# Kernel optimization log

Hardware: AMD Instinct MI355X
Metric: run time of the kernel (lower is better)

## Reference

```python
import jax, jax.numpy as jnp
import numpy as np

N, E = 50000, 800000
IN_CH, HID, OUT_CH = 128, 256, 40
L, R = 3, 16
EPS = 1e-12


def setup_inputs() -> dict:
    key = jax.random.key(0)
    ks = jax.random.split(key, 16)
    s = 0.05
    return {
        'x': jax.random.normal(ks[0], (N, IN_CH), jnp.float32),
        'edge_index': jax.random.randint(ks[1], (2, E), 0, N, dtype=jnp.int64),
        'W_in': jax.random.normal(ks[2], (IN_CH, HID), jnp.float32) * s,
        'b_in': jnp.zeros((HID,), jnp.float32),
        'centers': jax.random.normal(ks[3], (L, R, HID), jnp.float32),
        'log_sigma': jnp.zeros((L, R, HID), jnp.float32),
        'W_rule': jax.random.normal(ks[4], (L, R, HID, HID), jnp.float32) * s,
        'b_rule': jnp.zeros((L, R, HID), jnp.float32),
        'W_self': jax.random.normal(ks[5], (L, HID, HID), jnp.float32) * s,
        'b_self': jnp.zeros((L, HID), jnp.float32),
        'gamma': jnp.ones((L, HID), jnp.float32),
        'beta': jnp.zeros((L, HID), jnp.float32),
        'W_h1': jax.random.normal(ks[6], (HID, HID // 2), jnp.float32) * s,
        'b_h1': jnp.zeros((HID // 2,), jnp.float32),
        'W_h2': jax.random.normal(ks[7], (HID // 2, OUT_CH), jnp.float32) * s,
        'b_h2': jnp.zeros((OUT_CH,), jnp.float32),
    }


def membership(h, c, log_s):
    # Gaussian rule firing, expanded to matmuls to avoid [N,R,H] distance tensor
    inv_s2 = jnp.exp(-2.0 * log_s)                         # [R,H]
    d = (h * h) @ inv_s2.T - 2.0 * (h @ (c * inv_s2).T) \
        + jnp.sum(c * c * inv_s2, axis=-1)                 # [N,R]
    firing = jnp.exp(-0.5 * d)
    return firing / (jnp.sum(firing, axis=-1, keepdims=True) + EPS)


def fmpl(h, src, dst, c, log_s, W_r, b_r, W_s, b_s):
    n = h.shape[0]
    deg = jax.ops.segment_sum(jnp.ones(src.shape[0], h.dtype), dst, num_segments=n)
    agg = jax.ops.segment_sum(h[src], dst, num_segments=n) / jnp.clip(deg, 1.0)[:, None]
    mu = membership(h, c, log_s)                           # [N,R]
    per_rule = jnp.einsum('ni,rio->nro', agg, W_r) + b_r[None]  # [N,R,H]
    fuzzy = jnp.einsum('nr,nro->no', mu, per_rule)
    return h @ W_s + b_s + fuzzy


def batchnorm(x, g, b, eps=1e-5):
    m = jnp.mean(x, axis=0)
    v = jnp.var(x, axis=0)
    return (x - m) * jax.lax.rsqrt(v + eps) * g + b


def reference(x, edge_index, W_in, b_in, centers, log_sigma, W_rule, b_rule,
              W_self, b_self, gamma, beta, W_h1, b_h1, W_h2, b_h2):
    src, dst = edge_index[0], edge_index[1]
    h = jax.nn.relu(x @ W_in + b_in)                       # dropout = identity (eval)
    for l in range(L):
        h_new = fmpl(h, src, dst, centers[l], log_sigma[l], W_rule[l], b_rule[l],
                     W_self[l], b_self[l])
        h_new = jax.nn.relu(batchnorm(h_new, gamma[l], beta[l]))
        h = h + h_new
    logits = jax.nn.relu(h @ W_h1 + b_h1) @ W_h2 + b_h2
    return jax.nn.softmax(logits, axis=-1)
```

## Files before the change

kernel.cpp:

```cpp
#include <hip/hip_runtime.h>
#include <hip/hip_fp16.h>
#include <cstdint>
#include <cstddef>

using u16 = unsigned short;
using u32 = unsigned int;

typedef _Float16 half8 __attribute__((ext_vector_type(8)));
typedef float f32x4 __attribute__((ext_vector_type(4)));

static inline int cdiv(int a, int b) { return (a + b - 1) / b; }


__global__ void prep_k(const float* __restrict__ Wr,
                       const float* __restrict__ Ws, const float* __restrict__ br,
                       const float* __restrict__ W_in, const float* __restrict__ W_h1,
                       const float* __restrict__ W_h2,
                       const float* __restrict__ centers, const float* __restrict__ logsig,
                       u16* __restrict__ wcat,
                       u16* __restrict__ winp, u16* __restrict__ wh1p,
                       u16* __restrict__ wh2p,
                       u16* __restrict__ pcB, float* __restrict__ pccc,
                       int* __restrict__ zerobase, int nzero,
                       int Z, int Wb) {
    const int bid = blockIdx.x;
    const int tid = threadIdx.x;
    if (bid < Z) {
        int i = bid * 256 + tid;
        if (i < nzero) zerobase[i] = 0;
        return;
    }
    if (bid < Z + Wb) {
        size_t t = (size_t)(bid - Z) * 256 + tid;
        const size_t PL = 552u * 256u * 8u;
        int l = (int)(t / PL);
        size_t rem = t - (size_t)l * PL;
        int kp = (int)(rem >> 11);
        int o = (int)((rem >> 3) & 255);
        int e = (int)(rem & 7);
        int k = kp * 8 + e;
        float v;
        if (k < 4096)      v = Wr[((((size_t)l * 16 + (k >> 8)) * 256) + (k & 255)) * 256 + o];
        else if (k < 4352) v = Ws[(((size_t)l * 256) + (k - 4096)) * 256 + o];
        else if (k < 4368) v = br[(((size_t)l * 16) + (k - 4352)) * 256 + o];
        else               v = 0.f;
        union { u16 u; _Float16 h; } c; c.h = (_Float16)v;
        wcat[t] = c.u;
        return;
    }
    if (bid < Z + Wb + 128) {
        size_t t = (size_t)(bid - Z - Wb) * 256 + tid;
        int e = (int)(t & 7), o = (int)((t >> 3) & 255);
        int kp = (int)(t >> 11);
        union { u16 u; _Float16 h; } c; c.h = (_Float16)W_in[(size_t)(kp * 8 + e) * 256 + o];
        winp[t] = c.u;
        return;
    }
    if (bid < Z + Wb + 256) {
        size_t t = (size_t)(bid - Z - Wb - 128) * 256 + tid;
        int e = (int)(t & 7), o = (int)((t >> 3) & 127);
        int kp = (int)(t >> 10);
        union { u16 u; _Float16 h; } c; c.h = (_Float16)W_h1[(size_t)(kp * 8 + e) * 128 + o];
// ... 52 lines not shown
        for (int e = blockIdx.x * 256 + tid; e < E; e += 256 * 256)
            atomicAdd(&deg[dst[e]], 1);
        gbar(1);
        if (blockIdx.x == 0) {
            const int chunk = (n + 255) >> 8;
            int s0 = tid * chunk, s1 = s0 + chunk; if (s1 > n) s1 = n; if (s0 > n) s0 = n;
            int tot = 0;
            for (int i = s0; i < s1; ++i) tot += atomicAdd(&deg[i], 0);
            __shared__ int sm[256];
            sm[tid] = tot; __syncthreads();
            for (int off = 1; off < 256; off <<= 1) {
                int t = (tid >= off) ? sm[tid - off] : 0;
                __syncthreads(); sm[tid] += t; __syncthreads();
            }
            int base = sm[tid] - tot;
            for (int i = s0; i < s1; ++i) {
                int d = atomicAdd(&deg[i], 0);
                indptr[i] = base; cursor[i] = base;
                deginv[i] = 1.f / (float)(d > 1 ? d : 1);
                base += d;
            }
            if (tid == 255) indptr[n] = sm[255];
        }
        gbar(2);
        for (int e = blockIdx.x * 256 + tid; e < E; e += 256 * 256) {
            int d = dst[e];
            int pos = atomicAdd(&cursor[d], 1);
            ssrc[pos] = src[e];
        }
        gbar(3);
        if (blockIdx.x == 0 && tid == 0) *done = 1;
    }
    int lane = tid & 63, wave = tid >> 6;
    for (int node = blockIdx.x * 4 + wave; node < n; node += 256 * 4) {
        if (bflag[node >> 7] == 0) continue;
        int j0 = indptr[node], j1 = indptr[node + 1];
        float a0 = 0, a1 = 0, a2 = 0, a3 = 0;
        for (int j = j0; j < j1; ++j) {
            int sN = ssrc[j];
            union { uint2 u; _Float16 h[4]; } hv;
            hv.u = *(const uint2*)(h16 + (size_t)sN * 256 + lane * 4);
            a0 += (float)hv.h[0]; a1 += (float)hv.h[1];
            a2 += (float)hv.h[2]; a3 += (float)hv.h[3];
        }
        float di = deginv[node];
        union { uint2 u; _Float16 h[4]; } o;
        o.h[0] = (_Float16)(a0 * di); o.h[1] = (_Float16)(a1 * di);
        o.h[2] = (_Float16)(a2 * di); o.h[3] = (_Float16)(a3 * di);
        *(uint2*)(agg16 + (size_t)node * 256 + lane * 4) = o.u;
    }
}


template <int MODE, int NCHUNK>
__launch_bounds__(256, 2)
__global__ void gemm_mn(const u16* __restrict__ A, const u16* __restrict__ A2,
                        const u16* __restrict__ MU, const u16* __restrict__ Bp,
                        const float* __restrict__ bias, const int* __restrict__ bflag,
                        u16* __restrict__ outH, float* __restrict__ bnsum,
                        const u16* __restrict__ pcB, const float* __restrict__ pccc,
                        u16* __restrict__ mu16, int* __restrict__ bflagN,
                        int nrows) {
    __shared__ __align__(16) u16 lds[24576];
    __shared__ float bnbuf[2048];
    u16* lA = lds;
    u16* lB = lds + 8192;
    const int tid = threadIdx.x;
    const int row0 = blockIdx.x * 128;
    const int lane = tid & 63;
    const int q = lane >> 4, mm = lane & 15;
    const int wave = tid >> 6;

    f32x4 acc[2][16];
#pragma unroll
    for (int i = 0; i < 2; ++i)
#pragma unroll
        for (int j = 0; j < 16; ++j) acc[i][j] = (f32x4){0.f, 0.f, 0.f, 0.f};

    int cb = 0, cbEnd = NCHUNK;
    if (MODE == 1 && bflag[blockIdx.x] == 0) { cb = 64; cbEnd = 68; }

    for (; cb < cbEnd; ++cb) {
#pragma unroll
        for (int it = 0; it < 8; ++it) {
            int idx = it * 256 + tid;
            int p = idx >> 8, col = idx & 255;
            uint4 v = *(const uint4*)(Bp + (((size_t)(cb * 8 + p)) * 256 + col) * 8);
            *(uint4*)(lB + (size_t)idx * 8) = v;
        }
#pragma unroll
        for (int it = 0; it < 4; ++it) {
            int idx = it * 256 + tid;
            int p = idx >> 7, row = idx & 127;
            int grow = row0 + row; if (grow >= nrows) grow = nrows - 1;
            uint4 v;
            if (MODE == 0) {
                const float* xr = (const float*)A + (size_t)grow * 128 + cb * 64 + (p << 3);
                float4 f0 = *(const float4*)xr;
                float4 f1 = *(const float4*)(xr + 4);
                union { uint4 u4; _Float16 h[8]; } cv;
                cv.h[0] = (_Float16)f0.x; cv.h[1] = (_Float16)f0.y;
                cv.h[2] = (_Float16)f0.z; cv.h[3] = (_Float16)f0.w;
                cv.h[4] = (_Float16)f1.x; cv.h[5] = (_Float16)f1.y;
                cv.h[6] = (_Float16)f1.z; cv.h[7] = (_Float16)f1.w;
                v = cv.u4;
            } else {
                if (cb < 64) {
                    int r = cb >> 2;
                    int i0 = ((cb & 3) << 6) + (p << 3);
                    v = *(const uint4*)(A + (size_t)grow * 256 + i0);
                    union { u16 u; _Float16 h; } mu; mu.u = MU[(size_t)grow * 16 + r];
                    union { uint4 u4; _Float16 h[8]; } wv; wv.u4 = v;
#pragma unroll
                    for (int j = 0; j < 8; ++j) wv.h[j] = wv.h[j] * mu.h;
                    v = wv.u4;
                } else if (cb < 68) {
                    int i0 = ((cb - 64) << 6) + (p << 3);
                    v = *(const uint4*)(A2 + (size_t)grow * 256 + i0);
                } else {
                    int j0 = p << 3;
                    if (j0 < 16) v = *(const uint4*)(MU + (size_t)grow * 16 + j0);
                    else v = (uint4){0, 0, 0, 0};
                }
            }
            *(uint4*)(lA + (size_t)idx * 8) = v;
        }
        __syncthreads();
#pragma unroll
        for (int kc = 0; kc < 2; ++kc) {
            int pp = kc * 4 + q;
            half8 af0 = *(const half8*)(lA + ((size_t)pp * 128 + wave * 32 + mm) * 8);
            half8 af1 = *(const half8*)(lA + ((size_t)pp * 128 + wave * 32 + 16 + mm) * 8);
#pragma unroll
            for (int nt = 0; nt < 16; ++nt) {
                half8 bf = *(const half8*)(lB + ((size_t)pp * 256 + nt * 16 + mm) * 8);
                acc[0][nt] = __builtin_amdgcn_mfma_f32_16x16x32_f16(af0, bf, acc[0][nt], 0, 0, 0);
                acc[1][nt] = __builtin_amdgcn_mfma_f32_16x16x32_f16(af1, bf, acc[1][nt], 0, 0, 0);
            }
        }
        __syncthreads();
    }

    int nr = nrows - row0; if (nr > 128) nr = 128;

    if (MODE == 1) {
#pragma unroll
        for (int nt = 0; nt < 16; ++nt) {
            int cl = nt * 16 + mm;
            float bb = bias[cl];
            float s = 0.f, ss = 0.f;
#pragma unroll
            for (int mt = 0; mt < 2; ++mt) {
#pragma unroll
                for (int r = 0; r < 4; ++r) {
                    int row = wave * 32 + mt * 16 + q * 4 + r;
                    float v = acc[mt][nt][r] + bb;
                    if (row < nr) { s += v; ss += v * v; }
                }
            }
            s += __shfl_xor(s, 16);  s += __shfl_xor(s, 32);
            ss += __shfl_xor(ss, 16); ss += __shfl_xor(ss, 32);
            if (q == 0) {
                bnbuf[(wave * 256 + cl) * 2 + 0] = s;
                bnbuf[(wave * 256 + cl) * 2 + 1] = ss;
            }
        }
        __syncthreads();
        {
            float s  = bnbuf[tid * 2]     + bnbuf[(256 + tid) * 2]
                     + bnbuf[(512 + tid) * 2] + bnbuf[(768 + tid) * 2];
            float ss = bnbuf[tid * 2 + 1] + bnbuf[(256 + tid) * 2 + 1]
                     + bnbuf[(512 + tid) * 2 + 1] + bnbuf[(768 + tid) * 2 + 1];
            atomicAdd(&bnsum[tid], s);
            atomicAdd(&bnsum[256 + tid], ss);
        }
    }

    f32x4 macc0 = (f32x4){0.f, 0.f, 0.f, 0.f};
    f32x4 macc1 = (f32x4){0.f, 0.f, 0.f, 0.f};
#pragma unroll
    for (int h = 0; h < 2; ++h) {
        __syncthreads();
#pragma unroll
        for (int nt = 0; nt < 8; ++nt) {
            int cl = h * 128 + nt * 16 + mm;
            float bb = bias[cl];
#pragma unroll
            for (int mt = 0; mt < 2; ++mt) {
#pragma unroll
                for (int r = 0; r < 4; ++r) {
                    int row = wave * 32 + mt * 16 + q * 4 + r;
                    float v = acc[mt][h * 8 + nt][r] + bb;
                    if (MODE == 0) v = fmaxf(v, 0.f);
                    union { u16 u; _Float16 hh; } cc; cc.hh = (_Float16)v;
                    lds[row * 136 + nt * 16 + mm] = cc.u;
                }
            }
        }
        __syncthreads();
#pragma unroll
        for (int it = 0; it < 8; ++it) {
            int idx = it * 256 + tid;
            int row = idx >> 4, cp = idx & 15;
            if (row < nr) {
                uint4 v = *(const uint4*)(lds + row * 136 + cp * 8);
                *(uint4*)(outH + (size_t)(row0 + row) * 256 + h * 128 + cp * 8) = v;
            }
        }
        if (MODE == 0) {
            const u16* brow = pcB + (size_t)mm * 512;
#pragma unroll
            for (int it2 = 0; it2 < 4; ++it2) {
                int lk = it2 * 32 + q * 8;
                half8 b1 = *(const half8*)(brow + h * 128 + lk);
                half8 b2 = *(const half8*)(brow + 256 + h * 128 + lk);
                half8 a0 = *(const half8*)(lds + ((size_t)(wave * 32 + mm)) * 136 + lk);
                half8 a1 = *(const half8*)(lds + ((size_t)(wave * 32 + 16 + mm)) * 136 + lk);
                macc0 = __builtin_amdgcn_mfma_f32_16x16x32_f16(a0 * a0, b1, macc0, 0, 0, 0);
                macc0 = __builtin_amdgcn_mfma_f32_16x16x32_f16(a0, b2, macc0, 0, 0, 0);
                macc1 = __builtin_amdgcn_mfma_f32_16x16x32_f16(a1 * a1, b1, macc1, 0, 0, 0);
                macc1 = __builtin_amdgcn_mfma_f32_16x16x32_f16(a1, b2, macc1, 0, 0, 0);
            }
        }
    }

    if (MODE == 0) {
        float cc = pccc[mm];
        bool any = false;
#pragma unroll
        for (int g = 0; g < 2; ++g) {
            f32x4 macc = g ? macc1 : macc0;
#pragma unroll
            for (int r = 0; r < 4; ++r) {
                float d = macc[r] + cc;
                float f = expf(-0.5f * d);
                float s = f;
                s += __shfl_xor(s, 1); s += __shfl_xor(s, 2);
                s += __shfl_xor(s, 4); s += __shfl_xor(s, 8);
                int node = row0 + (wave * 2 + g) * 16 + q * 4 + r;
                if (node < nrows) {
                    union { u16 u; _Float16 hh; } c2;
                    c2.hh = (_Float16)(f / (s + 1e-12f));
                    mu16[(size_t)node * 16 + mm] = c2.u;
                    if (c2.u != 0) any = true;
                }
            }
        }
        if (__any(any) && lane == 0) {
            atomicOr(&bflagN[blockIdx.x], 1);
            atomicOr(&bflagN[511], 1);
        }
    }
}


template <int DOMEMB>
__launch_bounds__(256)
__global__ void updmemb_k(const u16* __restrict__ pre16, const float* __restrict__ bnsum,
                          const float* __restrict__ gamma, const float* __restrict__ beta,
                          u16* __restrict__ h16,
                          const u16* __restrict__ pcB, const float* __restrict__ pccc,
                          u16* __restrict__ mu16, int* __restrict__ bflag, int n) {
    const int tid = threadIdx.x;
    __shared__ float l_ab[512];
    {
        float su = bnsum[tid];
        float sq = bnsum[256 + tid];
        float invn = 1.f / (float)n;
        float m = su * invn;
        float al = gamma[tid] * rsqrtf(sq * invn - m * m + 1e-5f);
        l_ab[tid] = al;
        l_ab[256 + tid] = beta[tid] - m * al;
    }
    __syncthreads();

    const int lane = tid & 63, wave = tid >> 6;
    const int q = lane >> 4, mm = lane & 15;
    const int n0 = (blockIdx.x * 4 + wave) * 16;
    if (n0 >= n) return;
    const int node = n0 + mm;
    const bool valid = node < n;
    const int nodeC = valid ? node : n - 1;
    const size_t base = (size_t)nodeC * 256 + q * 8;

    half8 v16[8];
#pragma unroll
    for (int b = 0; b < 8; ++b) {
        int c = b * 32 + q * 8;
        float4 alA = *(const float4*)(l_ab + c);
        float4 alB = *(const float4*)(l_ab + c + 4);
        float4 shA = *(const float4*)(l_ab + 256 + c);
        float4 shB = *(const float4*)(l_ab + 256 + c + 4);
        float aarr[8] = {alA.x, alA.y, alA.z, alA.w, alB.x, alB.y, alB.z, alB.w};
        float harr[8] = {shA.x, shA.y, shA.z, shA.w, shB.x, shB.y, shB.z, shB.w};
        union { uint4 u; _Float16 hh[8]; } p, hv, o;
        p.u  = *(const uint4*)(pre16 + base + b * 32);
        hv.u = *(const uint4*)(h16 + base + b * 32);
#pragma unroll
        for (int j = 0; j < 8; ++j) {
            float v = (float)hv.hh[j] + fmaxf((float)p.hh[j] * aarr[j] + harr[j], 0.f);
            o.hh[j] = (_Float16)v;
        }
        if (valid) *(uint4*)(h16 + base + b * 32) = o.u;
        v16[b] = *(half8*)&o;
    }

    if (DOMEMB) {
        const u16* brow = pcB + (size_t)mm * 512;
        f32x4 acc = (f32x4){0.f, 0.f, 0.f, 0.f};
#pragma unroll
        for (int it = 0; it < 16; ++it) {
            half8 a = v16[it & 7];
            if (it < 8) a = a * a;
            half8 bb = *(const half8*)(brow + it * 32 + q * 8);
            acc = __builtin_amdgcn_mfma_f32_16x16x32_f16(a, bb, acc, 0, 0, 0);
        }
        float cc = pccc[mm];
        bool any = false;
#pragma unroll
        for (int r = 0; r < 4; ++r) {
            float d = acc[r] + cc;
            float f = expf(-0.5f * d);
            float s = f;
            s += __shfl_xor(s, 1); s += __shfl_xor(s, 2);
            s += __shfl_xor(s, 4); s += __shfl_xor(s, 8);
            int nd = n0 + q * 4 + r;
            if (nd < n) {
                union { u16 u; _Float16 h; } c2;
                c2.h = (_Float16)(f / (s + 1e-12f));
                mu16[(size_t)nd * 16 + mm] = c2.u;
                if (c2.u != 0) any = true;
            }
        }
        if (__any(any) && lane == 0) {
            atomicOr(&bflag[n0 >> 7], 1);
            atomicOr(&bflag[511], 1);
        }
    }
}


__launch_bounds__(256, 4)
__global__ void head_k(const u16* __restrict__ A, const u16* __restrict__ Bp,
                       const float* __restrict__ bias,
                       const u16* __restrict__ wh2, const float* __restrict__ bh2,
                       float* __restrict__ outF, int nrows) {
    __shared__ __align__(16) u16 lds[17408];
    u16* lA = lds;
    u16* lB = lds + 8192;
    const int tid = threadIdx.x;
    const int row0 = blockIdx.x * 128;
    const int lane = tid & 63;
    const int q = lane >> 4, mm = lane & 15;
    const int wave = tid >> 6;
    const int wm = wave >> 1, wn = wave & 1;

    f32x4 acc[4][4];
#pragma unroll
    for (int i = 0; i < 4; ++i)
#pragma unroll
        for (int j = 0; j < 4; ++j) acc[i][j] = (f32x4){0.f, 0.f, 0.f, 0.f};

    for (int cb = 0; cb < 4; ++cb) {
#pragma unroll
        for (int it = 0; it < 4; ++it) {
            int idx = it * 256 + tid;
            int p = idx >> 7, col = idx & 127;
            uint4 v = *(const uint4*)(Bp + (((size_t)(cb * 8 + p)) * 128 + col) * 8);
            *(uint4*)(lB + (size_t)idx * 8) = v;
        }
#pragma unroll
        for (int it = 0; it < 4; ++it) {
            int idx = it * 256 + tid;
            int p = idx >> 7, row = idx & 127;
            int grow = row0 + row; if (grow >= nrows) grow = nrows - 1;
            uint4 v = *(const uint4*)(A + (size_t)grow * 256 + cb * 64 + p * 8);
            *(uint4*)(lA + (size_t)idx * 8) = v;
        }
        __syncthreads();
#pragma unroll
        for (int kc = 0; kc < 2; ++kc) {
            int pp = kc * 4 + q;
            half8 af[4], bf[4];
#pragma unroll
            for (int mt = 0; mt < 4; ++mt)
                af[mt] = *(const half8*)(lA + ((size_t)pp * 128 + wm * 64 + mt * 16 + mm) * 8);
#pragma unroll
            for (int nt = 0; nt < 4; ++nt)
                bf[nt] = *(const half8*)(lB + ((size_t)pp * 128 + wn * 64 + nt * 16 + mm) * 8);
#pragma unroll
            for (int mt = 0; mt < 4; ++mt)
#pragma unroll
                for (int nt = 0; nt < 4; ++nt)
                    acc[mt][nt] = __builtin_amdgcn_mfma_f32_16x16x32_f16(af[mt], bf[nt], acc[mt][nt], 0, 0, 0);
        }
        __syncthreads();
    }

#pragma unroll
    for (int nt = 0; nt < 4; ++nt) {
        const int cl = wn * 64 + nt * 16 + mm;
#pragma unroll
        for (int mt = 0; mt < 4; ++mt) {
#pragma unroll
            for (int r = 0; r < 4; ++r) {
                int row = wm * 64 + mt * 16 + q * 4 + r;
                float v = fmaxf(acc[mt][nt][r] + bias[cl], 0.f);
                union { u16 u; _Float16 h; } cc; cc.h = (_Float16)v;
                lds[row * 136 + cl] = cc.u;
            }
        }
    }
    __syncthreads();

    const bool c2ok = (mm < 8);
    float b0 = bh2[mm], b1 = bh2[16 + mm];
    float b2 = c2ok ? bh2[32 + mm] : 0.f;
#pragma unroll
    for (int half = 0; half < 2; ++half) {
        int rbase = half * 64 + wave * 16;
        f32x4 hacc[3];
#pragma unroll
        for (int t = 0; t < 3; ++t) hacc[t] = (f32x4){0.f, 0.f, 0.f, 0.f};
#pragma unroll
        for (int c = 0; c < 4; ++c) {
            half8 a = *(const half8*)(lds + (rbase + mm) * 136 + c * 32 + q * 8);
#pragma unroll
            for (int t = 0; t < 3; ++t) {
                half8 b = *(const half8*)(wh2 + ((size_t)(c * 4 + q) * 48 + t * 16 + mm) * 8);
                hacc[t] = __builtin_amdgcn_mfma_f32_16x16x32_f16(a, b, hacc[t], 0, 0, 0);
            }
        }
#pragma unroll
        for (int r = 0; r < 4; ++r) {
            int node = row0 + rbase + q * 4 + r;
            float v0 = hacc[0][r] + b0;
            float v1 = hacc[1][r] + b1;
            float v2 = c2ok ? (hacc[2][r] + b2) : -3e38f;
            float m = fmaxf(fmaxf(v0, v1), v2);
            m = fmaxf(m, __shfl_xor(m, 1)); m = fmaxf(m, __shfl_xor(m, 2));
            m = fmaxf(m, __shfl_xor(m, 4)); m = fmaxf(m, __shfl_xor(m, 8));
            float e0 = expf(v0 - m), e1 = expf(v1 - m);
            float e2 = c2ok ? expf(v2 - m) : 0.f;
            float s = e0 + e1 + e2;
            s += __shfl_xor(s, 1); s += __shfl_xor(s, 2);
            s += __shfl_xor(s, 4); s += __shfl_xor(s, 8);
            float is = 1.f / s;
            if (node < nrows) {
                float* op = outF + (size_t)node * 40;
                op[mm] = e0 * is;
                op[16 + mm] = e1 * is;
                if (c2ok) op[32 + mm] = e2 * is;
            }
        }
    }
}


extern "C" void kernel_launch(void* const* d_in, const int* in_sizes, int n_in,
                              void* d_out, int out_size, void* d_ws, size_t ws_size,
                              hipStream_t stream) {
    const float* x       = (const float*)d_in[0];
    const int*   ei      = (const int*)d_in[1];
    const float* W_in    = (const float*)d_in[2];
    const float* b_in    = (const float*)d_in[3];
    const float* centers = (const float*)d_in[4];
    const float* logsig  = (const float*)d_in[5];
    const float* W_rule  = (const float*)d_in[6];
    const float* b_rule  = (const float*)d_in[7];
    const float* W_self  = (const float*)d_in[8];
    const float* b_self  = (const float*)d_in[9];
    const float* gamma   = (const float*)d_in[10];
    const float* beta    = (const float*)d_in[11];
    const float* W_h1    = (const float*)d_in[12];
    const float* b_h1    = (const float*)d_in[13];
    const float* W_h2    = (const float*)d_in[14];
    const float* b_h2    = (const float*)d_in[15];

    const int N = in_sizes[0] / 128;
    const int E = in_sizes[1] / 2;
    const int* e_src = ei;
    const int* e_dst = ei + E;

    char* w = (char*)d_ws;
    size_t off = 0;
    auto alloc = [&](size_t bytes) -> void* {
        void* p = w + off;
        off = (off + bytes + 255) & ~(size_t)255;
        return p;
    };

    const int gx = cdiv(N, 128);

    u16*   h16    = (u16*)  alloc((size_t)N * 256 * 2);
    u16*   pre16  = (u16*)  alloc((size_t)N * 256 * 2);
    u16*   agg16  = (u16*)  alloc((size_t)N * 256 * 2);
    u16*   mu16   = (u16*)  alloc((size_t)N * 16 * 2);
    u16*   wcat   = (u16*)  alloc((size_t)3 * 552 * 256 * 8 * 2);
    u16*   winp   = (u16*)  alloc((size_t)16 * 256 * 8 * 2);
    u16*   wh1p   = (u16*)  alloc((size_t)32 * 128 * 8 * 2);
    u16*   wh2p   = (u16*)  alloc((size_t)16 * 48 * 8 * 2);
    u16*   pcB    = (u16*)  alloc((size_t)48 * 512 * 2);
    float* pccc   = (float*)alloc((size_t)48 * 4);
    int*   indptr = (int*)  alloc((size_t)(N + 1) * 4);
    int*   cursor = (int*)  alloc((size_t)N * 4);
    float* deginv = (float*)alloc((size_t)N * 4);
    int*   ssrc   = (int*)  alloc((size_t)E * 4);
    const int nzero = N + 3 * 512 + 3 * 512 + 16;
    int*   zerob  = (int*)  alloc((size_t)nzero * 4);
    int*   deg    = zerob;
    int*   bflagA = zerob + N;
    float* bnsumA = (float*)(zerob + N + 3 * 512);
    int*   misc   = zerob + N + 3 * 512 + 3 * 512;
    int*   done   = misc;
    int*   csrctr = misc + 1;

    const int Z = cdiv(nzero, 256);
    const int Wb = 3 * 552 * 256 * 8 / 256;
    const int prep_grid = Z + Wb + 128 + 128 + 24 + 48;

    prep_k<<<prep_grid, 256, 0, stream>>>(W_rule, W_self, b_rule, W_in, W_h1, W_h2,
                                          centers, logsig, wcat, winp, wh1p, wh2p,
                                          pcB, pccc, zerob, nzero, Z, Wb);

    gemm_mn<0, 2><<<gx, 256, 0, stream>>>((const u16*)x, nullptr, nullptr, winp,
                                          b_in, nullptr, h16, nullptr,
                                          pcB, pccc, mu16, bflagA, N);

    for (int l = 0; l < 3; ++l) {
        int* bf = bflagA + l * 512;
        float* bns = bnsumA + l * 512;
        csr_agg_g<<<256, 256, 0, stream>>>(e_src, e_dst, deg, indptr, cursor, deginv,
                                           ssrc, csrctr, bf, done, h16, agg16, E, N);
        gemm_mn<1, 69><<<gx, 256, 0, stream>>>(agg16, h16, mu16,
                                               wcat + (size_t)l * 552 * 256 * 8,
                                               b_self + l * 256, bf, pre16, bns,
                                               nullptr, nullptr, nullptr, nullptr, N);
        if (l < 2) {
            updmemb_k<1><<<cdiv(N, 64), 256, 0, stream>>>(pre16, bns, gamma + l * 256,
                                                          beta + l * 256, h16,
                                                          pcB + (size_t)(l + 1) * 16 * 512,
                                                          pccc + (l + 1) * 16, mu16,
                                                          bflagA + (l + 1) * 512, N);
        } else {
            updmemb_k<0><<<cdiv(N, 64), 256, 0, stream>>>(pre16, bns, gamma + l * 256,
                                                          beta + l * 256, h16,
                                                          nullptr, nullptr, nullptr,
                                                          nullptr, N);
        }
    }

    head_k<<<gx, 256, 0, stream>>>(h16, wh1p, b_h1, wh2p, b_h2, (float*)d_out, N);
}
```

Before: 310.3 us.

## Drop LDS staging in fuzzy GEMM and fuse head MLP into last BN update

The main GEMM now has each wave load its A fragments straight from global memory and read B fragments directly from the pre-packed weights, with no shared-memory staging and no block barriers. LDS becomes a small per-wave tile used only for the epilogue, and occupancy is raised to three blocks per SM. The separate head kernel is removed, and the final batchnorm/residual kernel computes the two head matmuls and the softmax on its in-register tile, which also skips writing h back. The trade-off is that B is reloaded from global/L2 by every wave rather than shared through LDS, which adds memory traffic.

```diff
diff --git a/kernel.cpp b/kernel.cpp
--- a/kernel.cpp
+++ b/kernel.cpp
@@ -8,6 +8,8 @@
 
 typedef _Float16 half8 __attribute__((ext_vector_type(8)));
 typedef float f32x4 __attribute__((ext_vector_type(4)));
+
+#define MF(a, b, c) __builtin_amdgcn_mfma_f32_16x16x32_f16((a), (b), (c), 0, 0, 0)
 
 static inline int cdiv(int a, int b) { return (a + b - 1) / b; }
 
@@ -166,24 +168,24 @@
 }
 
 
-template <int MODE, int NCHUNK>
-__launch_bounds__(256, 2)
-__global__ void gemm_mn(const u16* __restrict__ A, const u16* __restrict__ A2,
-                        const u16* __restrict__ MU, const u16* __restrict__ Bp,
-                        const float* __restrict__ bias, const int* __restrict__ bflag,
-                        u16* __restrict__ outH, float* __restrict__ bnsum,
-                        const u16* __restrict__ pcB, const float* __restrict__ pccc,
-                        u16* __restrict__ mu16, int* __restrict__ bflagN,
-                        int nrows) {
-    __shared__ __align__(16) u16 lds[24576];
+template <int MODE>
+__launch_bounds__(256, 3)
+__global__ void gemm_d(const float* __restrict__ xf, const u16* __restrict__ hg,
+                       const u16* __restrict__ agg, const u16* __restrict__ mu,
+                       const u16* __restrict__ Bp, const float* __restrict__ bias,
+                       const int* __restrict__ bflag,
+                       u16* __restrict__ outH, float* __restrict__ bnl,
+                       const u16* __restrict__ pcB, const float* __restrict__ pccc,
+                       u16* __restrict__ mu16o, int* __restrict__ bflagN, int n) {
+    __shared__ __align__(16) u16 tiles[4][4352];
     __shared__ float bnbuf[2048];
-    u16* lA = lds;
-    u16* lB = lds + 8192;
-    const int tid = threadIdx.x;
-    const int row0 = blockIdx.x * 128;
-    const int lane = tid & 63;
-    const int q = lane >> 4, mm = lane & 15;
-    const int wave = tid >> 6;
+    const int tid = threadIdx.x, bid = blockIdx.x;
+    const int row0 = bid * 128;
+    const int lane = tid & 63, q = lane >> 4, mm = lane & 15, wave = tid >> 6;
+    u16* tw = tiles[wave];
+    int nr = n - row0; if (nr > 128) nr = 128;
+    int g0 = row0 + wave * 32 + mm;      if (g0 >= n) g0 = n - 1;
+    int g1 = row0 + wave * 32 + 16 + mm; if (g1 >= n) g1 = n - 1;
 
     f32x4 acc[2][16];
 #pragma unroll
@@ -191,25 +193,14 @@
 #pragma unroll
         for (int j = 0; j < 16; ++j) acc[i][j] = (f32x4){0.f, 0.f, 0.f, 0.f};
 
-    int cb = 0, cbEnd = NCHUNK;
-    if (MODE == 1 && bflag[blockIdx.x] == 0) { cb = 64; cbEnd = 68; }
-
-    for (; cb < cbEnd; ++cb) {
-#pragma unroll
-        for (int it = 0; it < 8; ++it) {
-            int idx = it * 256 + tid;
-            int p = idx >> 8, col = idx & 255;
-            uint4 v = *(const uint4*)(Bp + (((size_t)(cb * 8 + p)) * 256 + col) * 8);
-            *(uint4*)(lB + (size_t)idx * 8) = v;
-        }
-#pragma unroll
-        for (int it = 0; it < 4; ++it) {
-            int idx = it * 256 + tid;
-            int p = idx >> 7, row = idx & 127;
-            int grow = row0 + row; if (grow >= nrows) grow = nrows - 1;
-            uint4 v;
-            if (MODE == 0) {
-                const float* xr = (const float*)A + (size_t)grow * 128 + cb * 64 + (p << 3);
+    if (MODE == 0) {
+        for (int c = 0; c < 4; ++c) {
+#pragma unroll
+            for (int w2 = 0; w2 < 2; ++w2) {
+                int idx = w2 * 64 + lane;
+                int rl = idx >> 2, k8 = (idx & 3) * 8;
+                int grow = row0 + wave * 32 + rl; if (grow >= n) grow = n - 1;
+                const float* xr = xf + (size_t)grow * 128 + c * 32 + k8;
                 float4 f0 = *(const float4*)xr;
                 float4 f1 = *(const float4*)(xr + 4);
                 union { uint4 u4; _Float16 h[8]; } cv;
@@ -217,61 +208,83 @@
                 cv.h[2] = (_Float16)f0.z; cv.h[3] = (_Float16)f0.w;
                 cv.h[4] = (_Float16)f1.x; cv.h[5] = (_Float16)f1.y;
                 cv.h[6] = (_Float16)f1.z; cv.h[7] = (_Float16)f1.w;
-                v = cv.u4;
-            } else {
-                if (cb < 64) {
-                    int r = cb >> 2;
-                    int i0 = ((cb & 3) << 6) + (p << 3);
-                    v = *(const uint4*)(A + (size_t)grow * 256 + i0);
-                    union { u16 u; _Float16 h; } mu; mu.u = MU[(size_t)grow * 16 + r];
-                    union { uint4 u4; _Float16 h[8]; } wv; wv.u4 = v;
-#pragma unroll
-                    for (int j = 0; j < 8; ++j) wv.h[j] = wv.h[j] * mu.h;
-                    v = wv.u4;
-                } else if (cb < 68) {
-                    int i0 = ((cb - 64) << 6) + (p << 3);
-                    v = *(const uint4*)(A2 + (size_t)grow * 256 + i0);
-                } else {
-                    int j0 = p << 3;
-                    if (j0 < 16) v = *(const uint4*)(MU + (size_t)grow * 16 + j0);
-                    else v = (uint4){0, 0, 0, 0};
+                *(uint4*)(tw + rl * 32 + k8) = cv.u4;
+            }
+            half8 af0 = *(const half8*)(tw + mm * 32 + q * 8);
+            half8 af1 = *(const half8*)(tw + (16 + mm) * 32 + q * 8);
+            const u16* bp = Bp + ((size_t)(c * 4 + q) * 256 + mm) * 8;
+#pragma unroll
+            for (int nt = 0; nt < 16; ++nt) {
+                half8 bf = *(const half8*)(bp + nt * 128);
+                acc[0][nt] = MF(af0, bf, acc[0][nt]);
+                acc[1][nt] = MF(af1, bf, acc[1][nt]);
+            }
+        }
+    } else {
+        const bool fire = bflag[bid] != 0;
+        if (fire) {
+            const u16* ag0 = agg + (size_t)g0 * 256;
+            const u16* ag1 = agg + (size_t)g1 * 256;
+            for (int r = 0; r < 16; ++r) {
+                union { u16 u; _Float16 h; } m0u, m1u;
+                m0u.u = mu[(size_t)g0 * 16 + r];
+                m1u.u = mu[(size_t)g1 * 16 + r];
+                _Float16 m0 = m0u.h, m1 = m1u.h;
+#pragma unroll
+                for (int kf = 0; kf < 8; ++kf) {
+                    half8 af0 = *(const half8*)(ag0 + kf * 32 + q * 8) * m0;
+                    half8 af1 = *(const half8*)(ag1 + kf * 32 + q * 8) * m1;
+                    const u16* bp = Bp + ((size_t)((r * 32 + kf * 4 + q) * 256) + mm) * 8;
+#pragma unroll
+                    for (int nt = 0; nt < 16; ++nt) {
+                        half8 bf = *(const half8*)(bp + nt * 128);
+                        acc[0][nt] = MF(af0, bf, acc[0][nt]);
+                        acc[1][nt] = MF(af1, bf, acc[1][nt]);
+                    }
                 }
             }
-            *(uint4*)(lA + (size_t)idx * 8) = v;
-        }
-        __syncthreads();
-#pragma unroll
-        for (int kc = 0; kc < 2; ++kc) {
-            int pp = kc * 4 + q;
-            half8 af0 = *(const half8*)(lA + ((size_t)pp * 128 + wave * 32 + mm) * 8);
-            half8 af1 = *(const half8*)(lA + ((size_t)pp * 128 + wave * 32 + 16 + mm) * 8);
+        }
+#pragma unroll
+        for (int kf = 0; kf < 8; ++kf) {
+            half8 af0 = *(const half8*)(hg + (size_t)g0 * 256 + kf * 32 + q * 8);
+            half8 af1 = *(const half8*)(hg + (size_t)g1 * 256 + kf * 32 + q * 8);
+            const u16* bp = Bp + ((size_t)((512 + kf * 4 + q) * 256) + mm) * 8;
 #pragma unroll
             for (int nt = 0; nt < 16; ++nt) {
-                half8 bf = *(const half8*)(lB + ((size_t)pp * 256 + nt * 16 + mm) * 8);
-                acc[0][nt] = __builtin_amdgcn_mfma_f32_16x16x32_f16(af0, bf, acc[0][nt], 0, 0, 0);
-                acc[1][nt] = __builtin_amdgcn_mfma_f32_16x16x32_f16(af1, bf, acc[1][nt], 0, 0, 0);
-            }
-        }
-        __syncthreads();
-    }
-
-    int nr = nrows - row0; if (nr > 128) nr = 128;
-
-    if (MODE == 1) {
+                half8 bf = *(const half8*)(bp + nt * 128);
+                acc[0][nt] = MF(af0, bf, acc[0][nt]);
+                acc[1][nt] = MF(af1, bf, acc[1][nt]);
+            }
+        }
+        if (fire) {
+            half8 a0 = (half8){0, 0, 0, 0, 0, 0, 0, 0};
+            half8 a1 = (half8){0, 0, 0, 0, 0, 0, 0, 0};
+            if (q < 2) {
+                a0 = *(const half8*)(mu + (size_t)g0 * 16 + q * 8);
+                a1 = *(const half8*)(mu + (size_t)g1 * 16 + q * 8);
+            }
+            const u16* bp = Bp + ((size_t)((544 + q) * 256) + mm) * 8;
+#pragma unroll
+            for (int nt = 0; nt < 16; ++nt) {
+                half8 bf = *(const half8*)(bp + nt * 128);
+                acc[0][nt] = MF(a0, bf, acc[0][nt]);
+                acc[1][nt] = MF(a1, bf, acc[1][nt]);
+            }
+        }
+
 #pragma unroll
         for (int nt = 0; nt < 16; ++nt) {
             int cl = nt * 16 + mm;
             float bb = bias[cl];
             float s = 0.f, ss = 0.f;
 #pragma unroll
-            for (int mt = 0; mt < 2; ++mt) {
+            for (int mt = 0; mt < 2; ++mt)
 #pragma unroll
                 for (int r = 0; r < 4; ++r) {
-                    int row = wave * 32 + mt * 16 + q * 4 + r;
+                    int lrow = wave * 32 + mt * 16 + q * 4 + r;
                     float v = acc[mt][nt][r] + bb;
-                    if (row < nr) { s += v; ss += v * v; }
+                    if (lrow < nr) { s += v; ss += v * v; }
                 }
-            }
             s += __shfl_xor(s, 16);  s += __shfl_xor(s, 32);
             ss += __shfl_xor(ss, 16); ss += __shfl_xor(ss, 32);
             if (q == 0) {
@@ -281,12 +294,12 @@
         }
         __syncthreads();
         {
-            float s  = bnbuf[tid * 2]     + bnbuf[(256 + tid) * 2]
+            float s  = bnbuf[tid * 2]       + bnbuf[(256 + tid) * 2]
                      + bnbuf[(512 + tid) * 2] + bnbuf[(768 + tid) * 2];
-            float ss = bnbuf[tid * 2 + 1] + bnbuf[(256 + tid) * 2 + 1]
+            float ss = bnbuf[tid * 2 + 1]   + bnbuf[(256 + tid) * 2 + 1]
                      + bnbuf[(512 + tid) * 2 + 1] + bnbuf[(768 + tid) * 2 + 1];
-            atomicAdd(&bnsum[tid], s);
-            atomicAdd(&bnsum[256 + tid], ss);
+            atomicAdd(&bnl[tid], s);
+            atomicAdd(&bnl[256 + tid], ss);
         }
     }
 
@@ -294,32 +307,28 @@
     f32x4 macc1 = (f32x4){0.f, 0.f, 0.f, 0.f};
 #pragma unroll
     for (int h = 0; h < 2; ++h) {
-        __syncthreads();
 #pragma unroll
         for (int nt = 0; nt < 8; ++nt) {
             int cl = h * 128 + nt * 16 + mm;
             float bb = bias[cl];
 #pragma unroll
-            for (int mt = 0; mt < 2; ++mt) {
+            for (int mt = 0; mt < 2; ++mt)
 #pragma unroll
                 for (int r = 0; r < 4; ++r) {
-                    int row = wave * 32 + mt * 16 + q * 4 + r;
+                    int lrow = mt * 16 + q * 4 + r;
                     float v = acc[mt][h * 8 + nt][r] + bb;
                     if (MODE == 0) v = fmaxf(v, 0.f);
                     union { u16 u; _Float16 hh; } cc; cc.hh = (_Float16)v;
-                    lds[row * 136 + nt * 16 + mm] = cc.u;
+                    tw[lrow * 136 + nt * 16 + mm] = cc.u;
                 }
-            }
-        }
-        __syncthreads();
+        }
 #pragma unroll
         for (int it = 0; it < 8; ++it) {
-            int idx = it * 256 + tid;
+            int idx = it * 64 + lane;
             int row = idx >> 4, cp = idx & 15;
-            if (row < nr) {
-                uint4 v = *(const uint4*)(lds + row * 136 + cp * 8);
-                *(uint4*)(outH + (size_t)(row0 + row) * 256 + h * 128 + cp * 8) = v;
-            }
+            if (wave * 32 + row < nr)
+                *(uint4*)(outH + (size_t)(row0 + wave * 32 + row) * 256 + h * 128 + cp * 8) =
+                    *(const uint4*)(tw + row * 136 + cp * 8);
         }
         if (MODE == 0) {
             const u16* brow = pcB + (size_t)mm * 512;
@@ -328,55 +337,59 @@
                 int lk = it2 * 32 + q * 8;
                 half8 b1 = *(const half8*)(brow + h * 128 + lk);
                 half8 b2 = *(const half8*)(brow + 256 + h * 128 + lk);
-                half8 a0 = *(const half8*)(lds + ((size_t)(wave * 32 + mm)) * 136 + lk);
-                half8 a1 = *(const half8*)(lds + ((size_t)(wave * 32 + 16 + mm)) * 136 + lk);
-                macc0 = __builtin_amdgcn_mfma_f32_16x16x32_f16(a0 * a0, b1, macc0, 0, 0, 0);
-                macc0 = __builtin_amdgcn_mfma_f32_16x16x32_f16(a0, b2, macc0, 0, 0, 0);
-                macc1 = __builtin_amdgcn_mfma_f32_16x16x32_f16(a1 * a1, b1, macc1, 0, 0, 0);
-                macc1 = __builtin_amdgcn_mfma_f32_16x16x32_f16(a1, b2, macc1, 0, 0, 0);
+                half8 a0 = *(const half8*)(tw + (size_t)mm * 136 + lk);
+                half8 a1 = *(const half8*)(tw + (size_t)(16 + mm) * 136 + lk);
+                macc0 = MF(a0 * a0, b1, macc0);
+                macc0 = MF(a0, b2, macc0);
+                macc1 = MF(a1 * a1, b1, macc1);
+                macc1 = MF(a1, b2, macc1);
             }
         }
     }
 
     if (MODE == 0) {
-        float cc = pccc[mm];
+        float ccv = pccc[mm];
         bool any = false;
 #pragma unroll
         for (int g = 0; g < 2; ++g) {
             f32x4 macc = g ? macc1 : macc0;
 #pragma unroll
             for (int r = 0; r < 4; ++r) {
-                float d = macc[r] + cc;
+                float d = macc[r] + ccv;
                 float f = expf(-0.5f * d);
                 float s = f;
                 s += __shfl_xor(s, 1); s += __shfl_xor(s, 2);
                 s += __shfl_xor(s, 4); s += __shfl_xor(s, 8);
                 int node = row0 + (wave * 2 + g) * 16 + q * 4 + r;
-                if (node < nrows) {
+                if (node < n) {
                     union { u16 u; _Float16 hh; } c2;
                     c2.hh = (_Float16)(f / (s + 1e-12f));
-                    mu16[(size_t)node * 16 + mm] = c2.u;
+                    mu16o[(size_t)node * 16 + mm] = c2.u;
                     if (c2.u != 0) any = true;
                 }
             }
         }
         if (__any(any) && lane == 0) {
-            atomicOr(&bflagN[blockIdx.x], 1);
+            atomicOr(&bflagN[bid], 1);
             atomicOr(&bflagN[511], 1);
         }
     }
 }
 
 
-template <int DOMEMB>
+template <int TAIL>
 __launch_bounds__(256)
-__global__ void updmemb_k(const u16* __restrict__ pre16, const float* __restrict__ bnsum,
-                          const float* __restrict__ gamma, const float* __restrict__ beta,
-                          u16* __restrict__ h16,
-                          const u16* __restrict__ pcB, const float* __restrict__ pccc,
-                          u16* __restrict__ mu16, int* __restrict__ bflag, int n) {
+__global__ void upd_k(const u16* __restrict__ pre16, const float* __restrict__ bnsum,
+                      const float* __restrict__ gamma, const float* __restrict__ beta,
+                      u16* __restrict__ h16,
+                      const u16* __restrict__ pcB, const float* __restrict__ pccc,
+                      u16* __restrict__ mu16, int* __restrict__ bflag,
+                      const u16* __restrict__ wh1p, const float* __restrict__ bh1,
+                      const u16* __restrict__ wh2p, const float* __restrict__ bh2,
+                      float* __restrict__ outF, int n) {
     const int tid = threadIdx.x;
     __shared__ float l_ab[512];
+    __shared__ __align__(16) u16 qt[4][2176];
     {
         float su = bnsum[tid];
         float sq = bnsum[256 + tid];
@@ -415,11 +428,11 @@
             float v = (float)hv.hh[j] + fmaxf((float)p.hh[j] * aarr[j] + harr[j], 0.f);
             o.hh[j] = (_Float16)v;
         }
-        if (valid) *(uint4*)(h16 + base + b * 32) = o.u;
+        if (TAIL == 1 && valid) *(uint4*)(h16 + base + b * 32) = o.u;
         v16[b] = *(half8*)&o;
     }
 
-    if (DOMEMB) {
+    if (TAIL == 1) {
         const u16* brow = pcB + (size_t)mm * 512;
         f32x4 acc = (f32x4){0.f, 0.f, 0.f, 0.f};
 #pragma unroll
@@ -427,7 +440,7 @@
             half8 a = v16[it & 7];
             if (it < 8) a = a * a;
             half8 bb = *(const half8*)(brow + it * 32 + q * 8);
-            acc = __builtin_amdgcn_mfma_f32_16x16x32_f16(a, bb, acc, 0, 0, 0);
+            acc = MF(a, bb, acc);
         }
         float cc = pccc[mm];
         bool any = false;
@@ -451,103 +464,51 @@
             atomicOr(&bflag[511], 1);
         }
     }
-}
-
-
-__launch_bounds__(256, 4)
-__global__ void head_k(const u16* __restrict__ A, const u16* __restrict__ Bp,
-                       const float* __restrict__ bias,
-                       const u16* __restrict__ wh2, const float* __restrict__ bh2,
-                       float* __restrict__ outF, int nrows) {
-    __shared__ __align__(16) u16 lds[17408];
-    u16* lA = lds;
-    u16* lB = lds + 8192;
-    const int tid = threadIdx.x;
-    const int row0 = blockIdx.x * 128;
-    const int lane = tid & 63;
-    const int q = lane >> 4, mm = lane & 15;
-    const int wave = tid >> 6;
-    const int wm = wave >> 1, wn = wave & 1;
-
-    f32x4 acc[4][4];
-#pragma unroll
-    for (int i = 0; i < 4; ++i)
-#pragma unroll
-        for (int j = 0; j < 4; ++j) acc[i][j] = (f32x4){0.f, 0.f, 0.f, 0.f};
-
-    for (int cb = 0; cb < 4; ++cb) {
-#pragma unroll
-        for (int it = 0; it < 4; ++it) {
-            int idx = it * 256 + tid;
-            int p = idx >> 7, col = idx & 127;
-            uint4 v = *(const uint4*)(Bp + (((size_t)(cb * 8 + p)) * 128 + col) * 8);
-            *(uint4*)(lB + (size_t)idx * 8) = v;
-        }
-#pragma unroll
-        for (int it = 0; it < 4; ++it) {
-            int idx = it * 256 + tid;
-            int p = idx >> 7, row = idx & 127;
-            int grow = row0 + row; if (grow >= nrows) grow = nrows - 1;
-            uint4 v = *(const uint4*)(A + (size_t)grow * 256 + cb * 64 + p * 8);
-            *(uint4*)(lA + (size_t)idx * 8) = v;
-        }
-        __syncthreads();
-#pragma unroll
-        for (int kc = 0; kc < 2; ++kc) {
-            int pp = kc * 4 + q;
-            half8 af[4], bf[4];
-#pragma unroll
-            for (int mt = 0; mt < 4; ++mt)
-                af[mt] = *(const half8*)(lA + ((size_t)pp * 128 + wm * 64 + mt * 16 + mm) * 8);
-#pragma unroll
-            for (int nt = 0; nt < 4; ++nt)
-                bf[nt] = *(const half8*)(lB + ((size_t)pp * 128 + wn * 64 + nt * 16 + mm) * 8);
-#pragma unroll
-            for (int mt = 0; mt < 4; ++mt)
-#pragma unroll
-                for (int nt = 0; nt < 4; ++nt)
-                    acc[mt][nt] = __builtin_amdgcn_mfma_f32_16x16x32_f16(af[mt], bf[nt], acc[mt][nt], 0, 0, 0);
-        }
-        __syncthreads();
-    }
-
-#pragma unroll
-    for (int nt = 0; nt < 4; ++nt) {
-        const int cl = wn * 64 + nt * 16 + mm;
-#pragma unroll
-        for (int mt = 0; mt < 4; ++mt) {
+
+    if (TAIL == 2) {
+        u16* qw = qt[wave];
+        f32x4 hq[8];
+#pragma unroll
+        for (int j = 0; j < 8; ++j) hq[j] = (f32x4){0.f, 0.f, 0.f, 0.f};
+#pragma unroll
+        for (int b = 0; b < 8; ++b) {
+            half8 a = v16[b];
+            const u16* bp = wh1p + ((size_t)((b * 4 + q) * 128) + mm) * 8;
+#pragma unroll
+            for (int nt = 0; nt < 8; ++nt) {
+                half8 bf = *(const half8*)(bp + nt * 128);
+                hq[nt] = MF(a, bf, hq[nt]);
+            }
+        }
+#pragma unroll
+        for (int nt = 0; nt < 8; ++nt) {
+            int cl = nt * 16 + mm;
+            float bb = bh1[cl];
 #pragma unroll
             for (int r = 0; r < 4; ++r) {
-                int row = wm * 64 + mt * 16 + q * 4 + r;
-                float v = fmaxf(acc[mt][nt][r] + bias[cl], 0.f);
+                float v = fmaxf(hq[nt][r] + bb, 0.f);
                 union { u16 u; _Float16 h; } cc; cc.h = (_Float16)v;
-                lds[row * 136 + cl] = cc.u;
-            }
-        }
-    }
-    __syncthreads();
-
-    const bool c2ok = (mm < 8);
-    float b0 = bh2[mm], b1 = bh2[16 + mm];
-    float b2 = c2ok ? bh2[32 + mm] : 0.f;
-#pragma unroll
-    for (int half = 0; half < 2; ++half) {
-        int rbase = half * 64 + wave * 16;
+                qw[(q * 4 + r) * 136 + cl] = cc.u;
+            }
+        }
+        const bool c2ok = (mm < 8);
+        float b0 = bh2[mm], b1 = bh2[16 + mm];
+        float b2 = c2ok ? bh2[32 + mm] : 0.f;
         f32x4 hacc[3];
 #pragma unroll
         for (int t = 0; t < 3; ++t) hacc[t] = (f32x4){0.f, 0.f, 0.f, 0.f};
 #pragma unroll
         for (int c = 0; c < 4; ++c) {
-            half8 a = *(const half8*)(lds + (rbase + mm) * 136 + c * 32 + q * 8);
+            half8 a = *(const half8*)(qw + (size_t)mm * 136 + c * 32 + q * 8);
 #pragma unroll
             for (int t = 0; t < 3; ++t) {
-                half8 b = *(const half8*)(wh2 + ((size_t)(c * 4 + q) * 48 + t * 16 + mm) * 8);
-                hacc[t] = __builtin_amdgcn_mfma_f32_16x16x32_f16(a, b, hacc[t], 0, 0, 0);
+                half8 b = *(const half8*)(wh2p + ((size_t)(c * 4 + q) * 48 + t * 16 + mm) * 8);
+                hacc[t] = MF(a, b, hacc[t]);
             }
         }
 #pragma unroll
         for (int r = 0; r < 4; ++r) {
-            int node = row0 + rbase + q * 4 + r;
+            int nd = n0 + q * 4 + r;
             float v0 = hacc[0][r] + b0;
             float v1 = hacc[1][r] + b1;
             float v2 = c2ok ? (hacc[2][r] + b2) : -3e38f;
@@ -560,8 +521,8 @@
             s += __shfl_xor(s, 1); s += __shfl_xor(s, 2);
             s += __shfl_xor(s, 4); s += __shfl_xor(s, 8);
             float is = 1.f / s;
-            if (node < nrows) {
-                float* op = outF + (size_t)node * 40;
+            if (nd < n) {
+                float* op = outF + (size_t)nd * 40;
                 op[mm] = e0 * is;
                 op[16 + mm] = e1 * is;
                 if (c2ok) op[32 + mm] = e2 * is;
@@ -637,32 +598,33 @@
                                           centers, logsig, wcat, winp, wh1p, wh2p,
                                           pcB, pccc, zerob, nzero, Z, Wb);
 
-    gemm_mn<0, 2><<<gx, 256, 0, stream>>>((const u16*)x, nullptr, nullptr, winp,
-                                          b_in, nullptr, h16, nullptr,
-                                          pcB, pccc, mu16, bflagA, N);
+    gemm_d<0><<<gx, 256, 0, stream>>>(x, nullptr, nullptr, nullptr, winp, b_in,
+                                      nullptr, h16, nullptr, pcB, pccc, mu16,
+                                      bflagA, N);
 
     for (int l = 0; l < 3; ++l) {
         int* bf = bflagA + l * 512;
         float* bns = bnsumA + l * 512;
         csr_agg_g<<<256, 256, 0, stream>>>(e_src, e_dst, deg, indptr, cursor, deginv,
                                            ssrc, csrctr, bf, done, h16, agg16, E, N);
-        gemm_mn<1, 69><<<gx, 256, 0, stream>>>(agg16, h16, mu16,
-                                               wcat + (size_t)l * 552 * 256 * 8,
-                                               b_self + l * 256, bf, pre16, bns,
-                                               nullptr, nullptr, nullptr, nullptr, N);
+        gemm_d<1><<<gx, 256, 0, stream>>>(nullptr, h16, agg16, mu16,
+                                          wcat + (size_t)l * 552 * 256 * 8,
+                                          b_self + l * 256, bf, pre16, bns,
+                                          nullptr, nullptr, nullptr, nullptr, N);
         if (l < 2) {
-            updmemb_k<1><<<cdiv(N, 64), 256, 0, stream>>>(pre16, bns, gamma + l * 256,
-                                                          beta + l * 256, h16,
-                                                          pcB + (size_t)(l + 1) * 16 * 512,
-                                                          pccc + (l + 1) * 16, mu16,
-                                                          bflagA + (l + 1) * 512, N);
+            upd_k<1><<<cdiv(N, 64), 256, 0, stream>>>(pre16, bns, gamma + l * 256,
+                                                      beta + l * 256, h16,
+                                                      pcB + (size_t)(l + 1) * 16 * 512,
+                                                      pccc + (l + 1) * 16, mu16,
+                                                      bflagA + (l + 1) * 512,
+                                                      nullptr, nullptr, nullptr, nullptr,
+                                                      nullptr, N);
         } else {
-            updmemb_k<0><<<cdiv(N, 64), 256, 0, stream>>>(pre16, bns, gamma + l * 256,
-                                                          beta + l * 256, h16,
-                                                          nullptr, nullptr, nullptr,
-                                                          nullptr, N);
-        }
-    }
-
-    head_k<<<gx, 256, 0, stream>>>(h16, wh1p, b_h1, wh2p, b_h2, (float*)d_out, N);
+            upd_k<2><<<cdiv(N, 64), 256, 0, stream>>>(pre16, bns, gamma + l * 256,
+                                                      beta + l * 256, h16,
+                                                      nullptr, nullptr, nullptr, nullptr,
+                                                      wh1p, b_h1, wh2p, b_h2,
+                                                      (float*)d_out, N);
+        }
+    }
 }
```

New measurement: 401.1 us. 29.3% more time.

## Fuse classifier head into final residual/batchnorm update kernel

Applied to the files above, without the earlier changes.

The last layer's update kernel now runs the two-layer MLP head and softmax directly on the freshly computed fp16 hidden rows held in registers, with a per-wave LDS tile for the intermediate activations. This removes the separate head kernel launch, the final h16 write, and the re-read of h16. In exchange, each wave reads the W_h1 fragments straight from global memory instead of sharing them through LDS across a 128-row tile, and the kernel carries extra shared memory that may lower occupancy.

```diff
diff --git a/kernel.cpp b/kernel.cpp
--- a/kernel.cpp
+++ b/kernel.cpp
@@ -8,6 +8,8 @@
 
 typedef _Float16 half8 __attribute__((ext_vector_type(8)));
 typedef float f32x4 __attribute__((ext_vector_type(4)));
+
+#define MF(a, b, c) __builtin_amdgcn_mfma_f32_16x16x32_f16((a), (b), (c), 0, 0, 0)
 
 static inline int cdiv(int a, int b) { return (a + b - 1) / b; }
 
@@ -248,8 +250,8 @@
 #pragma unroll
             for (int nt = 0; nt < 16; ++nt) {
                 half8 bf = *(const half8*)(lB + ((size_t)pp * 256 + nt * 16 + mm) * 8);
-                acc[0][nt] = __builtin_amdgcn_mfma_f32_16x16x32_f16(af0, bf, acc[0][nt], 0, 0, 0);
-                acc[1][nt] = __builtin_amdgcn_mfma_f32_16x16x32_f16(af1, bf, acc[1][nt], 0, 0, 0);
+                acc[0][nt] = MF(af0, bf, acc[0][nt]);
+                acc[1][nt] = MF(af1, bf, acc[1][nt]);
             }
         }
         __syncthreads();
@@ -330,10 +332,10 @@
                 half8 b2 = *(const half8*)(brow + 256 + h * 128 + lk);
                 half8 a0 = *(const half8*)(lds + ((size_t)(wave * 32 + mm)) * 136 + lk);
                 half8 a1 = *(const half8*)(lds + ((size_t)(wave * 32 + 16 + mm)) * 136 + lk);
-                macc0 = __builtin_amdgcn_mfma_f32_16x16x32_f16(a0 * a0, b1, macc0, 0, 0, 0);
-                macc0 = __builtin_amdgcn_mfma_f32_16x16x32_f16(a0, b2, macc0, 0, 0, 0);
-                macc1 = __builtin_amdgcn_mfma_f32_16x16x32_f16(a1 * a1, b1, macc1, 0, 0, 0);
-                macc1 = __builtin_amdgcn_mfma_f32_16x16x32_f16(a1, b2, macc1, 0, 0, 0);
+                macc0 = MF(a0 * a0, b1, macc0);
+                macc0 = MF(a0, b2, macc0);
+                macc1 = MF(a1 * a1, b1, macc1);
+                macc1 = MF(a1, b2, macc1);
             }
         }
     }
@@ -368,15 +370,19 @@
 }
 
 
-template <int DOMEMB>
+template <int TAIL>
 __launch_bounds__(256)
-__global__ void updmemb_k(const u16* __restrict__ pre16, const float* __restrict__ bnsum,
-                          const float* __restrict__ gamma, const float* __restrict__ beta,
-                          u16* __restrict__ h16,
-                          const u16* __restrict__ pcB, const float* __restrict__ pccc,
-                          u16* __restrict__ mu16, int* __restrict__ bflag, int n) {
+__global__ void upd_k(const u16* __restrict__ pre16, const float* __restrict__ bnsum,
+                      const float* __restrict__ gamma, const float* __restrict__ beta,
+                      u16* __restrict__ h16,
+                      const u16* __restrict__ pcB, const float* __restrict__ pccc,
+                      u16* __restrict__ mu16, int* __restrict__ bflag,
+                      const u16* __restrict__ wh1p, const float* __restrict__ bh1,
+                      const u16* __restrict__ wh2p, const float* __restrict__ bh2,
+                      float* __restrict__ outF, int n) {
     const int tid = threadIdx.x;
     __shared__ float l_ab[512];
+    __shared__ __align__(16) u16 qt[4][2176];
     {
         float su = bnsum[tid];
         float sq = bnsum[256 + tid];
@@ -415,11 +421,11 @@
             float v = (float)hv.hh[j] + fmaxf((float)p.hh[j] * aarr[j] + harr[j], 0.f);
             o.hh[j] = (_Float16)v;
         }
-        if (valid) *(uint4*)(h16 + base + b * 32) = o.u;
+        if (TAIL == 1 && valid) *(uint4*)(h16 + base + b * 32) = o.u;
         v16[b] = *(half8*)&o;
     }
 
-    if (DOMEMB) {
+    if (TAIL == 1) {
         const u16* brow = pcB + (size_t)mm * 512;
         f32x4 acc = (f32x4){0.f, 0.f, 0.f, 0.f};
 #pragma unroll
@@ -427,7 +433,7 @@
             half8 a = v16[it & 7];
             if (it < 8) a = a * a;
             half8 bb = *(const half8*)(brow + it * 32 + q * 8);
-            acc = __builtin_amdgcn_mfma_f32_16x16x32_f16(a, bb, acc, 0, 0, 0);
+            acc = MF(a, bb, acc);
         }
         float cc = pccc[mm];
         bool any = false;
@@ -451,103 +457,51 @@
             atomicOr(&bflag[511], 1);
         }
     }
-}
-
-
-__launch_bounds__(256, 4)
-__global__ void head_k(const u16* __restrict__ A, const u16* __restrict__ Bp,
-                       const float* __restrict__ bias,
-                       const u16* __restrict__ wh2, const float* __restrict__ bh2,
-                       float* __restrict__ outF, int nrows) {
-    __shared__ __align__(16) u16 lds[17408];
-    u16* lA = lds;
-    u16* lB = lds + 8192;
-    const int tid = threadIdx.x;
-    const int row0 = blockIdx.x * 128;
-    const int lane = tid & 63;
-    const int q = lane >> 4, mm = lane & 15;
-    const int wave = tid >> 6;
-    const int wm = wave >> 1, wn = wave & 1;
-
-    f32x4 acc[4][4];
-#pragma unroll
-    for (int i = 0; i < 4; ++i)
-#pragma unroll
-        for (int j = 0; j < 4; ++j) acc[i][j] = (f32x4){0.f, 0.f, 0.f, 0.f};
-
-    for (int cb = 0; cb < 4; ++cb) {
-#pragma unroll
-        for (int it = 0; it < 4; ++it) {
-            int idx = it * 256 + tid;
-            int p = idx >> 7, col = idx & 127;
-            uint4 v = *(const uint4*)(Bp + (((size_t)(cb * 8 + p)) * 128 + col) * 8);
-            *(uint4*)(lB + (size_t)idx * 8) = v;
-        }
-#pragma unroll
-        for (int it = 0; it < 4; ++it) {
-            int idx = it * 256 + tid;
-            int p = idx >> 7, row = idx & 127;
-            int grow = row0 + row; if (grow >= nrows) grow = nrows - 1;
-            uint4 v = *(const uint4*)(A + (size_t)grow * 256 + cb * 64 + p * 8);
-            *(uint4*)(lA + (size_t)idx * 8) = v;
-        }
-        __syncthreads();
-#pragma unroll
-        for (int kc = 0; kc < 2; ++kc) {
-            int pp = kc * 4 + q;
-            half8 af[4], bf[4];
-#pragma unroll
-            for (int mt = 0; mt < 4; ++mt)
-                af[mt] = *(const half8*)(lA + ((size_t)pp * 128 + wm * 64 + mt * 16 + mm) * 8);
-#pragma unroll
-            for (int nt = 0; nt < 4; ++nt)
-                bf[nt] = *(const half8*)(lB + ((size_t)pp * 128 + wn * 64 + nt * 16 + mm) * 8);
-#pragma unroll
-            for (int mt = 0; mt < 4; ++mt)
-#pragma unroll
-                for (int nt = 0; nt < 4; ++nt)
-                    acc[mt][nt] = __builtin_amdgcn_mfma_f32_16x16x32_f16(af[mt], bf[nt], acc[mt][nt], 0, 0, 0);
-        }
-        __syncthreads();
-    }
-
-#pragma unroll
-    for (int nt = 0; nt < 4; ++nt) {
-        const int cl = wn * 64 + nt * 16 + mm;
-#pragma unroll
-        for (int mt = 0; mt < 4; ++mt) {
+
+    if (TAIL == 2) {
+        u16* qw = qt[wave];
+        f32x4 hq[8];
+#pragma unroll
+        for (int j = 0; j < 8; ++j) hq[j] = (f32x4){0.f, 0.f, 0.f, 0.f};
+#pragma unroll
+        for (int b = 0; b < 8; ++b) {
+            half8 a = v16[b];
+            const u16* bp = wh1p + ((size_t)((b * 4 + q) * 128) + mm) * 8;
+#pragma unroll
+            for (int nt = 0; nt < 8; ++nt) {
+                half8 bf = *(const half8*)(bp + nt * 128);
+                hq[nt] = MF(a, bf, hq[nt]);
+            }
+        }
+#pragma unroll
+        for (int nt = 0; nt < 8; ++nt) {
+            int cl = nt * 16 + mm;
+            float bb = bh1[cl];
 #pragma unroll
             for (int r = 0; r < 4; ++r) {
-                int row = wm * 64 + mt * 16 + q * 4 + r;
-                float v = fmaxf(acc[mt][nt][r] + bias[cl], 0.f);
+                float v = fmaxf(hq[nt][r] + bb, 0.f);
                 union { u16 u; _Float16 h; } cc; cc.h = (_Float16)v;
-                lds[row * 136 + cl] = cc.u;
-            }
-        }
-    }
-    __syncthreads();
-
-    const bool c2ok = (mm < 8);
-    float b0 = bh2[mm], b1 = bh2[16 + mm];
-    float b2 = c2ok ? bh2[32 + mm] : 0.f;
-#pragma unroll
-    for (int half = 0; half < 2; ++half) {
-        int rbase = half * 64 + wave * 16;
+                qw[(q * 4 + r) * 136 + cl] = cc.u;
+            }
+        }
+        const bool c2ok = (mm < 8);
+        float b0 = bh2[mm], b1 = bh2[16 + mm];
+        float b2 = c2ok ? bh2[32 + mm] : 0.f;
         f32x4 hacc[3];
 #pragma unroll
         for (int t = 0; t < 3; ++t) hacc[t] = (f32x4){0.f, 0.f, 0.f, 0.f};
 #pragma unroll
         for (int c = 0; c < 4; ++c) {
-            half8 a = *(const half8*)(lds + (rbase + mm) * 136 + c * 32 + q * 8);
+            half8 a = *(const half8*)(qw + (size_t)mm * 136 + c * 32 + q * 8);
 #pragma unroll
             for (int t = 0; t < 3; ++t) {
-                half8 b = *(const half8*)(wh2 + ((size_t)(c * 4 + q) * 48 + t * 16 + mm) * 8);
-                hacc[t] = __builtin_amdgcn_mfma_f32_16x16x32_f16(a, b, hacc[t], 0, 0, 0);
+                half8 b = *(const half8*)(wh2p + ((size_t)(c * 4 + q) * 48 + t * 16 + mm) * 8);
+                hacc[t] = MF(a, b, hacc[t]);
             }
         }
 #pragma unroll
         for (int r = 0; r < 4; ++r) {
-            int node = row0 + rbase + q * 4 + r;
+            int nd = n0 + q * 4 + r;
             float v0 = hacc[0][r] + b0;
             float v1 = hacc[1][r] + b1;
             float v2 = c2ok ? (hacc[2][r] + b2) : -3e38f;
@@ -560,8 +514,8 @@
             s += __shfl_xor(s, 1); s += __shfl_xor(s, 2);
             s += __shfl_xor(s, 4); s += __shfl_xor(s, 8);
             float is = 1.f / s;
-            if (node < nrows) {
-                float* op = outF + (size_t)node * 40;
+            if (nd < n) {
+                float* op = outF + (size_t)nd * 40;
                 op[mm] = e0 * is;
                 op[16 + mm] = e1 * is;
                 if (c2ok) op[32 + mm] = e2 * is;
@@ -651,18 +605,19 @@
                                                b_self + l * 256, bf, pre16, bns,
                                                nullptr, nullptr, nullptr, nullptr, N);
         if (l < 2) {
-            updmemb_k<1><<<cdiv(N, 64), 256, 0, stream>>>(pre16, bns, gamma + l * 256,
-                                                          beta + l * 256, h16,
-                                                          pcB + (size_t)(l + 1) * 16 * 512,
-                                                          pccc + (l + 1) * 16, mu16,
-                                                          bflagA + (l + 1) * 512, N);
+            upd_k<1><<<cdiv(N, 64), 256, 0, stream>>>(pre16, bns, gamma + l * 256,
+                                                      beta + l * 256, h16,
+                                                      pcB + (size_t)(l + 1) * 16 * 512,
+                                                      pccc + (l + 1) * 16, mu16,
+                                                      bflagA + (l + 1) * 512,
+                                                      nullptr, nullptr, nullptr, nullptr,
+                                                      nullptr, N);
         } else {
-            updmemb_k<0><<<cdiv(N, 64), 256, 0, stream>>>(pre16, bns, gamma + l * 256,
-                                                          beta + l * 256, h16,
-                                                          nullptr, nullptr, nullptr,
-                                                          nullptr, N);
-        }
-    }
-
-    head_k<<<gx, 256, 0, stream>>>(h16, wh1p, b_h1, wh2p, b_h2, (float*)d_out, N);
+            upd_k<2><<<cdiv(N, 64), 256, 0, stream>>>(pre16, bns, gamma + l * 256,
+                                                      beta + l * 256, h16,
+                                                      nullptr, nullptr, nullptr, nullptr,
+                                                      wh1p, b_h1, wh2p, b_h2,
+                                                      (float*)d_out, N);
+        }
+    }
 }
```

Measured after the change: 293.6 us. -5.4%, faster.
